# Kernel tuning notes

Hardware: AMD Instinct MI355X
Metric: run time of the kernel (lower is better)

The kernel has to match this reference:

```python
import jax, jax.numpy as jnp
import numpy as np

EMBED_DIM = 512
NUM_HEADS = 8
HEAD_DIM = EMBED_DIM // NUM_HEADS
PAIR_DIM = 64
B, L = 2, 1024


def setup_inputs() -> dict:
    key = jax.random.key(0)
    ks = jax.random.split(key, 6)
    seq_repr = jax.random.normal(ks[0], (B, L, EMBED_DIM), dtype=jnp.float32)
    pair_repr = jax.random.normal(ks[1], (B, L, L, PAIR_DIM), dtype=jnp.float32)
    # Parameters (stored as [in, out] for x @ W)
    sc = 0.02
    W_qkv = jax.random.normal(ks[2], (EMBED_DIM, 3 * EMBED_DIM), dtype=jnp.float32) * sc
    W_bias = jax.random.normal(ks[3], (PAIR_DIM, NUM_HEADS), dtype=jnp.float32) * sc
    W_out = jax.random.normal(ks[4], (EMBED_DIM, EMBED_DIM), dtype=jnp.float32) * sc
    b_out = jax.random.normal(ks[5], (EMBED_DIM,), dtype=jnp.float32) * sc
    return {"seq_repr": seq_repr, "pair_repr": pair_repr,
            "W_qkv": W_qkv, "W_bias": W_bias, "W_out": W_out, "b_out": b_out}


def reference(seq_repr, pair_repr, W_qkv, W_bias, W_out, b_out):
    b, l, _ = seq_repr.shape
    # pair bias: [B, L, L, pair_dim] -> [B, H, L, L]
    pair_bias = jnp.einsum('bijp,ph->bhij', pair_repr, W_bias)
    qkv = seq_repr @ W_qkv                      # [B, L, 3*E]
    q, k, v = jnp.split(qkv, 3, axis=-1)
    def heads(x):
        return x.reshape(b, l, NUM_HEADS, HEAD_DIM).transpose(0, 2, 1, 3)  # [B,H,L,D]
    q, k, v = heads(q), heads(k), heads(v)
    scale = 1.0 / jnp.sqrt(jnp.asarray(HEAD_DIM, dtype=q.dtype))
    scores = jnp.einsum('bhid,bhjd->bhij', q, k) * scale + pair_bias
    attn = jax.nn.softmax(scores, axis=-1)
    ctx = jnp.einsum('bhij,bhjd->bhid', attn, v)             # [B,H,L,D]
    ctx = ctx.transpose(0, 2, 1, 3).reshape(b, l, EMBED_DIM)
    return ctx @ W_out + b_out
```

## Files before the change

### kernel.cpp

```cpp
#include <hip/hip_runtime.h>
#include <hip/hip_bf16.h>


typedef __attribute__((ext_vector_type(8))) short bf16x8;
typedef __attribute__((ext_vector_type(4))) float f32x4;

#define BFLO(u) __uint_as_float(((unsigned)(u)) << 16)

__device__ __forceinline__ unsigned pk2(float a, float b) {
    __hip_bfloat16 ha = __float2bfloat16(a);
    __hip_bfloat16 hb = __float2bfloat16(b);
    return (unsigned)__bfloat16_as_ushort(ha) | ((unsigned)__bfloat16_as_ushort(hb) << 16);
}

__device__ __forceinline__ void gl16_nt(const void* g, void* l) {
    __builtin_amdgcn_global_load_lds((const __attribute__((address_space(1))) void*)g,
                                     (__attribute__((address_space(3))) void*)l, 16, 0, 2);
}

__global__ __launch_bounds__(256, 2) void gemm_qkv_kernel(
    const float* __restrict__ A, const float* __restrict__ W,
    unsigned short* __restrict__ qbus, unsigned short* __restrict__ kbus,
    unsigned short* __restrict__ vtbus)
{
    __shared__ float smem[64 * 68];
    float* As = smem;
    float* Bs = smem + 32 * 68;

    const int t  = threadIdx.x;
    const int m0 = blockIdx.y * 64;
    const int n0 = blockIdx.x * 64;
    const int tx = t & 15, ty = t >> 4;

    const int am = t >> 2, ak = (t & 3) * 8;
    const int bk = t >> 3, bn = (t & 7) * 8;

    float acc[4][4] = {};

    for (int k0 = 0; k0 < 512; k0 += 32) {
        float4 a0 = *(const float4*)&A[(size_t)(m0 + am) * 512 + k0 + ak];
        float4 a1 = *(const float4*)&A[(size_t)(m0 + am) * 512 + k0 + ak + 4];
        float4 b0 = *(const float4*)&W[(size_t)(k0 + bk) * 1536 + n0 + bn];
        float4 b1 = *(const float4*)&W[(size_t)(k0 + bk) * 1536 + n0 + bn + 4];
        __syncthreads();
        As[(ak + 0) * 68 + am] = a0.x;
        As[(ak + 1) * 68 + am] = a0.y;
        As[(ak + 2) * 68 + am] = a0.z;
        As[(ak + 3) * 68 + am] = a0.w;
        As[(ak + 4) * 68 + am] = a1.x;
        As[(ak + 5) * 68 + am] = a1.y;
        As[(ak + 6) * 68 + am] = a1.z;
        As[(ak + 7) * 68 + am] = a1.w;
        *(float4*)&Bs[bk * 68 + bn]     = b0;
        *(float4*)&Bs[bk * 68 + bn + 4] = b1;
        __syncthreads();
#pragma unroll
        for (int kk = 0; kk < 32; kk++) {
            float4 a4 = *(float4*)&As[kk * 68 + ty * 4];
            float4 b4 = *(float4*)&Bs[kk * 68 + tx * 4];
            float av[4] = {a4.x, a4.y, a4.z, a4.w};
            float bv[4] = {b4.x, b4.y, b4.z, b4.w};
#pragma unroll
            for (int r = 0; r < 4; r++)
#pragma unroll
                for (int c = 0; c < 4; c++) acc[r][c] += av[r] * bv[c];
        }
    }

    const int sect = n0 >> 9;
    const int h    = (n0 >> 6) & 7;
    const int b    = m0 >> 10;
    const int i0   = m0 & 1023;

    if (sect == 2) {
        __syncthreads();
        float* T = smem;
#pragma unroll
        for (int r = 0; r < 4; r++)
#pragma unroll
            for (int c = 0; c < 4; c++)
                T[(tx * 4 + c) * 68 + (ty * 4 + r)] = acc[r][c];
        __syncthreads();
        const int dp = t >> 2, iq = (t & 3) * 16;
        unsigned short* dst = vtbus + (((size_t)(b * 8 + h)) * 64 + dp) * 1024 + i0 + iq;
#pragma unroll
        for (int u = 0; u < 4; u++) {
            float4 f = *(float4*)&T[dp * 68 + iq + u * 4];
            uint2 pkd; pkd.x = pk2(f.x, f.y); pkd.y = pk2(f.z, f.w);
            *(uint2*)&dst[u * 4] = pkd;
        }
    } else {
        unsigned short* dst = (sect == 0) ? qbus : kbus;
        const float sc = (sect == 0) ? 0.125f : 1.0f;
#pragma unroll
        for (int r = 0; r < 4; r++) {
            const int i = i0 + ty * 4 + r;
#pragma unroll
            for (int c = 0; c < 4; c += 2) {
                unsigned u = pk2(acc[r][c] * sc, acc[r][c + 1] * sc);
                *(unsigned*)&dst[(((size_t)(b * 8 + h)) * 1024 + i) * 64 + tx * 4 + c] = u;
            }
        }
    }
}

__device__ __forceinline__ bf16x8 slab_frag(const char* rowb, int ks, int q4, int sw) {
    const int s0 = ks * 8 + q4 * 2;
    const float4 fa = *(const float4*)(rowb + (((s0    ) ^ sw) << 4));
    const float4 fb = *(const float4*)(rowb + (((s0 + 1) ^ sw) << 4));
    uint4 u;
    u.x = pk2(fa.x, fa.y); u.y = pk2(fa.z, fa.w);
    u.z = pk2(fb.x, fb.y); u.w = pk2(fb.z, fb.w);
    return *(bf16x8*)&u;
}

__global__ __launch_bounds__(512, 4) void attn_kernel(
    const float* __restrict__ pair, const float* __restrict__ Wb,
    const unsigned short* __restrict__ qbus, const unsigned short* __restrict__ kbus,
    const unsigned short* __restrict__ vtbus, float* __restrict__ cp,
    float* __restrict__ mlm, float* __restrict__ mll)
{
    __shared__ __align__(16) char plds[2][32768];
    __shared__ __align__(16) unsigned short bias_lds[128 * 17];
    __shared__ __align__(16) unsigned short pbuf[8 * 16 * 24];

    const int t    = threadIdx.x;
    const int lane = t & 63;
    const int w    = t >> 6;
    const int q4   = lane >> 4;
    const int l15  = lane & 15;

    const int bx   = blockIdx.x;
    const int vbid = ((bx & 7) << 6) | (bx >> 3);
    const int b    = vbid >> 8;
    const int rem  = vbid & 255;
    const int jh   = rem >> 7;
    const int i0   = (rem & 127) * 8;

    uint4 wbf[2];
#pragma unroll
    for (int ks = 0; ks < 2; ks++) {
        float f[8];
#pragma unroll
        for (int e = 0; e < 8; e++)
            f[e] = (l15 < 8) ? Wb[(ks * 32 + q4 * 8 + e) * 8 + l15] : 0.f;
        wbf[ks].x = pk2(f[0], f[1]); wbf[ks].y = pk2(f[2], f[3]);
        wbf[ks].z = pk2(f[4], f[5]); wbf[ks].w = pk2(f[6], f[7]);
    }

    uint4 qf[2] = {};
    if (l15 < 8) {
        const unsigned short* qrow = qbus + (size_t)((b * 8 + w) * 1024 + i0 + l15) * 64;
#pragma unroll
        for (int ks = 0; ks < 2; ks++)
            qf[ks] = *(const uint4*)(qrow + ks * 32 + q4 * 8);
    }

    asm volatile("s_waitcnt vmcnt(0)" ::: "memory");
    __builtin_amdgcn_sched_barrier(0);

    const char* prow = (const char*)pair
                     + ((size_t)(b * 1024 + i0 + w) * 1024 + jh * 512) * 256;
    int soff[4];
#pragma unroll
    for (int r = 0; r < 4; r++) {
        const int jl = r * 4 + q4;
        soff[r] = jl * 256 + ((l15 ^ jl) << 4);
    }
    char* ldsW = (char*)plds + w * 4096;

#define STAGE(bufsel, jtn) do {                                         \
        const char* gg = prow + (size_t)(jtn) * 4096;                   \
        char* ld = ldsW + (bufsel) * 32768;                             \
        _Pragma("unroll")                                               \
        for (int r = 0; r < 4; r++)                                     \
            gl16_nt(gg + soff[r], ld + r * 1024);                       \
    } while (0)

    STAGE(0, 0);

    f32x4 acc[4];
#pragma unroll
    for (int dn = 0; dn < 4; dn++) acc[dn] = (f32x4){0.f, 0.f, 0.f, 0.f};
    float mrun[4], lrun[4];
#pragma unroll
    for (int rr = 0; rr < 4; rr++) { mrun[rr] = -3.0e38f; lrun[rr] = 0.f; }

    const unsigned short* kbase = kbus + (size_t)((b * 8 + w) * 1024 + jh * 512) * 64;
    const unsigned short* vbase = vtbus + (size_t)((b * 8 + w) * 64) * 1024 + jh * 512;

#pragma unroll 1
    for (int jt = 0; jt < 32; jt++) {
        const char* cur = (const char*)plds + (jt & 1) * 32768;

        uint4 kf[2], vf[4];
        {
            const unsigned short* kt = kbase + (size_t)(jt * 16 + l15) * 64;
            kf[0] = *(const uint4*)(kt + q4 * 8);
            kf[1] = *(const uint4*)(kt + 32 + q4 * 8);
#pragma unroll
            for (int dn = 0; dn < 4; dn++)
                vf[dn] = *(const uint4*)(vbase + (size_t)(dn * 16 + l15) * 1024
                                         + jt * 16 + (q4 & 1) * 8);
        }

        if (jt < 31) {
            STAGE((jt + 1) & 1, jt + 1);
            asm volatile("s_waitcnt vmcnt(10)" ::: "memory");
        } else {
            asm volatile("s_waitcnt vmcnt(6)" ::: "memory");
        }
        __builtin_amdgcn_sched_barrier(0);

        {
            const char* rowb = cur + w * 4096 + l15 * 256;
            f32x4 bb = {0.f, 0.f, 0.f, 0.f};
#pragma unroll
            for (int ks = 0; ks < 2; ks++)
                bb = __builtin_amdgcn_mfma_f32_16x16x32_bf16(
                        slab_frag(rowb, ks, q4, l15), *(bf16x8*)&wbf[ks], bb, 0, 0, 0);
            if (l15 < 8) {
#pragma unroll
                for (int rr = 0; rr < 4; rr++)
                    bias_lds[(w * 16 + q4 * 4 + rr) * 17 + l15] =
                        __bfloat16_as_ushort(__float2bfloat16(bb[rr]));
            }
        }

        asm volatile("s_waitcnt lgkmcnt(0)" ::: "memory");
        __builtin_amdgcn_sched_barrier(0);
        __builtin_amdgcn_s_barrier();
        __builtin_amdgcn_sched_barrier(0);

        f32x4 s;
#pragma unroll
        for (int rr = 0; rr < 4; rr++) {
            const int ii = q4 * 4 + rr;
            s[rr] = (q4 < 2) ? BFLO(bias_lds[(ii * 16 + l15) * 17 + w]) : 0.f;
        }
        s = __builtin_amdgcn_mfma_f32_16x16x32_bf16(*(bf16x8*)&qf[0], *(bf16x8*)&kf[0], s, 0, 0, 0);
        s = __builtin_amdgcn_mfma_f32_16x16x32_bf16(*(bf16x8*)&qf[1], *(bf16x8*)&kf[1], s, 0, 0, 0);

#pragma unroll
        for (int rr = 0; rr < 4; rr++) {
            float x = s[rr];
            x = fmaxf(x, __shfl_xor(x, 1));
            x = fmaxf(x, __shfl_xor(x, 2));
            x = fmaxf(x, __shfl_xor(x, 4));
            x = fmaxf(x, __shfl_xor(x, 8));
            const float mnew = fmaxf(mrun[rr], x);
            const float corr = __expf(mrun[rr] - mnew);
            mrun[rr] = mnew;
            const float p0 = __expf(s[rr] - mnew);
            float ts = p0;
            ts += __shfl_xor(ts, 1);
            ts += __shfl_xor(ts, 2);
            ts += __shfl_xor(ts, 4);
            ts += __shfl_xor(ts, 8);
            lrun[rr] = lrun[rr] * corr + ts;
#pragma unroll
            for (int dn = 0; dn < 4; dn++) acc[dn][rr] *= corr;
            pbuf[(w * 16 + q4 * 4 + rr) * 24 + l15] =
                __bfloat16_as_ushort(__float2bfloat16(p0));
        }

        asm volatile("s_waitcnt lgkmcnt(0)" ::: "memory");
        __builtin_amdgcn_sched_barrier(0);

        bf16x8 pfrag = (bf16x8){0, 0, 0, 0, 0, 0, 0, 0};
        if (q4 < 2) pfrag = *(bf16x8*)&pbuf[(w * 16 + l15) * 24 + q4 * 8];
#pragma unroll
        for (int dn = 0; dn < 4; dn++)
            acc[dn] = __builtin_amdgcn_mfma_f32_16x16x32_bf16(pfrag, *(bf16x8*)&vf[dn], acc[dn], 0, 0, 0);

        __builtin_amdgcn_s_barrier();
    }

    if (q4 < 2) {
#pragma unroll
        for (int rr = 0; rr < 4; rr++) {
            const int i = q4 * 4 + rr;
            float* crow = cp + (size_t)jh * (2048 * 512)
                        + ((size_t)(b * 1024) + i0 + i) * 512 + w * 64;
#pragma unroll
            for (int dn = 0; dn < 4; dn++)
                crow[dn * 16 + l15] = acc[dn][rr];
            if (l15 == 0) {
                const int mi = ((jh * 2 + b) * 8 + w) * 1024 + i0 + i;
                mlm[mi] = mrun[rr];
                mll[mi] = lrun[rr];
            }
        }
    }
#undef STAGE
}

__global__ __launch_bounds__(256, 2) void gemm_out_fused(
    const float* __restrict__ cp, const float* __restrict__ mlm,
    const float* __restrict__ mll, const float* __restrict__ W,
    const float* __restrict__ bias, float* __restrict__ out)
{
    __shared__ float smem[64 * 68];
    float* As = smem;
    float* Bs = smem + 32 * 68;

    const int t  = threadIdx.x;
    const int m0 = blockIdx.y * 64;
    const int n0 = blockIdx.x * 64;
    const int tx = t & 15, ty = t >> 4;

    const int am = t >> 2, ak = (t & 3) * 8;
    const int bk = t >> 3, bn = (t & 7) * 8;

    const int row = m0 + am;
    const int bb  = row >> 10, ii = row & 1023;
    const float* cp0 = cp + (size_t)row * 512;
    const float* cp1 = cp + (size_t)(2048 * 512) + (size_t)row * 512;

    float acc[4][4] = {};
    float w0 = 0.f, w1 = 0.f;

    for (int k0 = 0; k0 < 512; k0 += 32) {
        if ((k0 & 63) == 0) {
            const int h   = k0 >> 6;
            const int mi0 = ((bb) * 8 + h) * 1024 + ii;
            const int mi1 = ((2 + bb) * 8 + h) * 1024 + ii;
            const float m0_ = mlm[mi0], m1_ = mlm[mi1];
            const float l0_ = mll[mi0], l1_ = mll[mi1];
            const float M   = fmaxf(m0_, m1_);
            float e0 = __expf(m0_ - M), e1 = __expf(m1_ - M);
            const float inv = 1.0f / (l0_ * e0 + l1_ * e1);
            w0 = e0 * inv; w1 = e1 * inv;
        }
        float4 c0a = *(const float4*)&cp0[k0 + ak];
        float4 c0b = *(const float4*)&cp0[k0 + ak + 4];
        float4 c1a = *(const float4*)&cp1[k0 + ak];
        float4 c1b = *(const float4*)&cp1[k0 + ak + 4];
        float4 b0 = *(const float4*)&W[(size_t)(k0 + bk) * 512 + n0 + bn];
        float4 b1 = *(const float4*)&W[(size_t)(k0 + bk) * 512 + n0 + bn + 4];
        float a0x = c0a.x * w0 + c1a.x * w1, a0y = c0a.y * w0 + c1a.y * w1;
        float a0z = c0a.z * w0 + c1a.z * w1, a0w = c0a.w * w0 + c1a.w * w1;
        float a1x = c0b.x * w0 + c1b.x * w1, a1y = c0b.y * w0 + c1b.y * w1;
        float a1z = c0b.z * w0 + c1b.z * w1, a1w = c0b.w * w0 + c1b.w * w1;
        __syncthreads();
        As[(ak + 0) * 68 + am] = a0x;
        As[(ak + 1) * 68 + am] = a0y;
        As[(ak + 2) * 68 + am] = a0z;
        As[(ak + 3) * 68 + am] = a0w;
        As[(ak + 4) * 68 + am] = a1x;
        As[(ak + 5) * 68 + am] = a1y;
        As[(ak + 6) * 68 + am] = a1z;
        As[(ak + 7) * 68 + am] = a1w;
        *(float4*)&Bs[bk * 68 + bn]     = b0;
        *(float4*)&Bs[bk * 68 + bn + 4] = b1;
        __syncthreads();
#pragma unroll
        for (int kk = 0; kk < 32; kk++) {
            float4 a4 = *(float4*)&As[kk * 68 + ty * 4];
            float4 b4 = *(float4*)&Bs[kk * 68 + tx * 4];
            float av[4] = {a4.x, a4.y, a4.z, a4.w};
            float bv[4] = {b4.x, b4.y, b4.z, b4.w};
#pragma unroll
            for (int r = 0; r < 4; r++)
#pragma unroll
                for (int c = 0; c < 4; c++) acc[r][c] += av[r] * bv[c];
        }
    }

    float4 bo = *(const float4*)&bias[n0 + tx * 4];
    float bv[4] = {bo.x, bo.y, bo.z, bo.w};
#pragma unroll
    for (int r = 0; r < 4; r++) {
        const int m = m0 + ty * 4 + r;
#pragma unroll
        for (int c = 0; c < 4; c++)
            out[(size_t)m * 512 + n0 + tx * 4 + c] = acc[r][c] + bv[c];
    }
}

extern "C" void kernel_launch(void* const* d_in, const int* in_sizes, int n_in,
                              void* d_out, int out_size, void* d_ws, size_t ws_size,
                              hipStream_t stream)
{
    const float* seq  = (const float*)d_in[0];
    const float* pair = (const float*)d_in[1];
    const float* Wqkv = (const float*)d_in[2];
    const float* Wb   = (const float*)d_in[3];
    const float* Wout = (const float*)d_in[4];
    const float* bout = (const float*)d_in[5];
    float* out = (float*)d_out;

    unsigned short* qbus  = (unsigned short*)d_ws;
    unsigned short* kbus  = qbus + (1 << 20);
    unsigned short* vtbus = kbus + (1 << 20);
    float*          cp    = (float*)(vtbus + (1 << 20));
    float*          mlm   = cp + (2 << 20);
    float*          mll   = mlm + (1 << 15);

    gemm_qkv_kernel<<<dim3(24, 32), 256, 0, stream>>>(seq, Wqkv, qbus, kbus, vtbus);
    attn_kernel<<<512, 512, 0, stream>>>(pair, Wb, qbus, kbus, vtbus, cp, mlm, mll);
    gemm_out_fused<<<dim3(8, 32), 256, 0, stream>>>(cp, mlm, mll, Wout, bout, out);
}
```

Measured before the change: 239.3 us.

## Use bf16 MFMA for QKV projection and pipeline pair-bias computation one tile ahead

Adds a prep kernel that converts seq to bf16 and transposes W_qkv into bf16 [N,K] layout. The QKV GEMM is rewritten to use 16x16x32 bf16 MFMA loading fragments straight from global memory, replacing the fp32 FMA LDS-tiled loop. The attention kernel now stages pair tiles two steps ahead and computes the pair bias for the next tile into a double-buffered LDS slot, which removes one barrier per iteration. The costs are an extra kernel launch with a conversion pass, more workspace, and lower precision in the projection.

```diff
diff --git a/kernel.cpp b/kernel.cpp
--- a/kernel.cpp
+++ b/kernel.cpp
@@ -18,53 +18,83 @@
                                      (__attribute__((address_space(3))) void*)l, 16, 0, 2);
 }
 
-__global__ __launch_bounds__(256, 2) void gemm_qkv_kernel(
-    const float* __restrict__ A, const float* __restrict__ W,
+__global__ __launch_bounds__(256) void prep_kernel(
+    const float* __restrict__ seq, const float* __restrict__ W,
+    unsigned short* __restrict__ seqb, unsigned short* __restrict__ wtb)
+{
+    __shared__ float T[64 * 68];
+    const int bx = blockIdx.x, t = threadIdx.x;
+    if (bx < 512) {
+        const size_t idx = ((size_t)bx * 256 + t) * 8;
+        float4 f0 = *(const float4*)&seq[idx];
+        float4 f1 = *(const float4*)&seq[idx + 4];
+        uint4 u;
+        u.x = pk2(f0.x, f0.y); u.y = pk2(f0.z, f0.w);
+        u.z = pk2(f1.x, f1.y); u.w = pk2(f1.z, f1.w);
+        *(uint4*)&seqb[idx] = u;
+    } else {
+        const int bb = bx - 512;
+        const int n0 = (bb % 24) * 64, k0 = (bb / 24) * 64;
+        const int kk = t >> 2, nch = (t & 3) * 16;
+#pragma unroll
+        for (int u = 0; u < 4; u++) {
+            float4 f = *(const float4*)&W[(size_t)(k0 + kk) * 1536 + n0 + nch + u * 4];
+            T[kk * 68 + nch + u * 4 + 0] = f.x;
+            T[kk * 68 + nch + u * 4 + 1] = f.y;
+            T[kk * 68 + nch + u * 4 + 2] = f.z;
+            T[kk * 68 + nch + u * 4 + 3] = f.w;
+        }
+        __syncthreads();
+        const int nn = t >> 2, kch = (t & 3) * 16;
+#pragma unroll
+        for (int u = 0; u < 4; u++) {
+            float a = T[(kch + u * 4 + 0) * 68 + nn];
+            float b = T[(kch + u * 4 + 1) * 68 + nn];
+            float c = T[(kch + u * 4 + 2) * 68 + nn];
+            float d = T[(kch + u * 4 + 3) * 68 + nn];
+            uint2 p; p.x = pk2(a, b); p.y = pk2(c, d);
+            *(uint2*)&wtb[(size_t)(n0 + nn) * 512 + k0 + kch + u * 4] = p;
+        }
+    }
+}
+
+__global__ __launch_bounds__(256) void gemm_qkv_kernel(
+    const unsigned short* __restrict__ seqb, const unsigned short* __restrict__ wtb,
     unsigned short* __restrict__ qbus, unsigned short* __restrict__ kbus,
     unsigned short* __restrict__ vtbus)
 {
-    __shared__ float smem[64 * 68];
-    float* As = smem;
-    float* Bs = smem + 32 * 68;
-
-    const int t  = threadIdx.x;
+    const int t    = threadIdx.x;
+    const int lane = t & 63;
+    const int wv   = t >> 6;
+    const int q4   = lane >> 4;
+    const int l15  = lane & 15;
+    const int mw   = wv >> 1, nw = wv & 1;
+
     const int m0 = blockIdx.y * 64;
     const int n0 = blockIdx.x * 64;
-    const int tx = t & 15, ty = t >> 4;
-
-    const int am = t >> 2, ak = (t & 3) * 8;
-    const int bk = t >> 3, bn = (t & 7) * 8;
-
-    float acc[4][4] = {};
-
+
+    f32x4 acc[2][2];
+#pragma unroll
+    for (int a = 0; a < 2; a++)
+#pragma unroll
+        for (int b = 0; b < 2; b++) acc[a][b] = (f32x4){0.f, 0.f, 0.f, 0.f};
+
+    const unsigned short* arow0 = seqb + (size_t)(m0 + mw * 32 + l15) * 512 + q4 * 8;
+    const unsigned short* brow0 = wtb + (size_t)(n0 + nw * 32 + l15) * 512 + q4 * 8;
+
+#pragma unroll 4
     for (int k0 = 0; k0 < 512; k0 += 32) {
-        float4 a0 = *(const float4*)&A[(size_t)(m0 + am) * 512 + k0 + ak];
-        float4 a1 = *(const float4*)&A[(size_t)(m0 + am) * 512 + k0 + ak + 4];
-        float4 b0 = *(const float4*)&W[(size_t)(k0 + bk) * 1536 + n0 + bn];
-        float4 b1 = *(const float4*)&W[(size_t)(k0 + bk) * 1536 + n0 + bn + 4];
-        __syncthreads();
-        As[(ak + 0) * 68 + am] = a0.x;
-        As[(ak + 1) * 68 + am] = a0.y;
-        As[(ak + 2) * 68 + am] = a0.z;
-        As[(ak + 3) * 68 + am] = a0.w;
-        As[(ak + 4) * 68 + am] = a1.x;
-        As[(ak + 5) * 68 + am] = a1.y;
-        As[(ak + 6) * 68 + am] = a1.z;
-        As[(ak + 7) * 68 + am] = a1.w;
-        *(float4*)&Bs[bk * 68 + bn]     = b0;
-        *(float4*)&Bs[bk * 68 + bn + 4] = b1;
-        __syncthreads();
-#pragma unroll
-        for (int kk = 0; kk < 32; kk++) {
-            float4 a4 = *(float4*)&As[kk * 68 + ty * 4];
-            float4 b4 = *(float4*)&Bs[kk * 68 + tx * 4];
-            float av[4] = {a4.x, a4.y, a4.z, a4.w};
-            float bv[4] = {b4.x, b4.y, b4.z, b4.w};
-#pragma unroll
-            for (int r = 0; r < 4; r++)
-#pragma unroll
-                for (int c = 0; c < 4; c++) acc[r][c] += av[r] * bv[c];
-        }
+        uint4 af[2], bf[2];
+        af[0] = *(const uint4*)(arow0 + k0);
+        af[1] = *(const uint4*)(arow0 + 16 * 512 + k0);
+        bf[0] = *(const uint4*)(brow0 + k0);
+        bf[1] = *(const uint4*)(brow0 + 16 * 512 + k0);
+#pragma unroll
+        for (int sm = 0; sm < 2; sm++)
+#pragma unroll
+            for (int sn = 0; sn < 2; sn++)
+                acc[sm][sn] = __builtin_amdgcn_mfma_f32_16x16x32_bf16(
+                    *(bf16x8*)&af[sm], *(bf16x8*)&bf[sn], acc[sm][sn], 0, 0, 0);
     }
 
     const int sect = n0 >> 9;
@@ -72,33 +102,24 @@
     const int b    = m0 >> 10;
     const int i0   = m0 & 1023;
 
-    if (sect == 2) {
-        __syncthreads();
-        float* T = smem;
-#pragma unroll
-        for (int r = 0; r < 4; r++)
-#pragma unroll
-            for (int c = 0; c < 4; c++)
-                T[(tx * 4 + c) * 68 + (ty * 4 + r)] = acc[r][c];
-        __syncthreads();
-        const int dp = t >> 2, iq = (t & 3) * 16;
-        unsigned short* dst = vtbus + (((size_t)(b * 8 + h)) * 64 + dp) * 1024 + i0 + iq;
-#pragma unroll
-        for (int u = 0; u < 4; u++) {
-            float4 f = *(float4*)&T[dp * 68 + iq + u * 4];
-            uint2 pkd; pkd.x = pk2(f.x, f.y); pkd.y = pk2(f.z, f.w);
-            *(uint2*)&dst[u * 4] = pkd;
-        }
-    } else {
-        unsigned short* dst = (sect == 0) ? qbus : kbus;
-        const float sc = (sect == 0) ? 0.125f : 1.0f;
-#pragma unroll
-        for (int r = 0; r < 4; r++) {
-            const int i = i0 + ty * 4 + r;
-#pragma unroll
-            for (int c = 0; c < 4; c += 2) {
-                unsigned u = pk2(acc[r][c] * sc, acc[r][c + 1] * sc);
-                *(unsigned*)&dst[(((size_t)(b * 8 + h)) * 1024 + i) * 64 + tx * 4 + c] = u;
+#pragma unroll
+    for (int sm = 0; sm < 2; sm++) {
+#pragma unroll
+        for (int sn = 0; sn < 2; sn++) {
+            const int d  = nw * 32 + sn * 16 + l15;
+            const int ib = i0 + mw * 32 + sm * 16 + q4 * 4;
+            if (sect == 2) {
+                uint2 p;
+                p.x = pk2(acc[sm][sn][0], acc[sm][sn][1]);
+                p.y = pk2(acc[sm][sn][2], acc[sm][sn][3]);
+                *(uint2*)&vtbus[(((size_t)(b * 8 + h)) * 64 + d) * 1024 + ib] = p;
+            } else {
+                unsigned short* dst = (sect == 0) ? qbus : kbus;
+                const float sc = (sect == 0) ? 0.125f : 1.0f;
+#pragma unroll
+                for (int rr = 0; rr < 4; rr++)
+                    dst[(((size_t)(b * 8 + h)) * 1024 + ib + rr) * 64 + d] =
+                        __bfloat16_as_ushort(__float2bfloat16(acc[sm][sn][rr] * sc));
             }
         }
     }
@@ -121,7 +142,7 @@
     float* __restrict__ mlm, float* __restrict__ mll)
 {
     __shared__ __align__(16) char plds[2][32768];
-    __shared__ __align__(16) unsigned short bias_lds[128 * 17];
+    __shared__ __align__(16) unsigned short bias_lds[2][128 * 17];
     __shared__ __align__(16) unsigned short pbuf[8 * 16 * 24];
 
     const int t    = threadIdx.x;
@@ -177,7 +198,32 @@
             gl16_nt(gg + soff[r], ld + r * 1024);                       \
     } while (0)
 
+#define BIASCOMP(pbsel, slot) do {                                      \
+        const char* rowb = (const char*)plds + (pbsel) * 32768          \
+                         + w * 4096 + l15 * 256;                        \
+        f32x4 bb = {0.f, 0.f, 0.f, 0.f};                                \
+        _Pragma("unroll")                                               \
+        for (int ks = 0; ks < 2; ks++)                                  \
+            bb = __builtin_amdgcn_mfma_f32_16x16x32_bf16(               \
+                    slab_frag(rowb, ks, q4, l15), *(bf16x8*)&wbf[ks],   \
+                    bb, 0, 0, 0);                                       \
+        if (l15 < 8) {                                                  \
+            _Pragma("unroll")                                           \
+            for (int rr = 0; rr < 4; rr++)                              \
+                bias_lds[slot][(w * 16 + q4 * 4 + rr) * 17 + l15] =     \
+                    __bfloat16_as_ushort(__float2bfloat16(bb[rr]));     \
+        }                                                               \
+    } while (0)
+
     STAGE(0, 0);
+    STAGE(1, 1);
+    asm volatile("s_waitcnt vmcnt(4)" ::: "memory");
+    __builtin_amdgcn_sched_barrier(0);
+    BIASCOMP(0, 0);
+    asm volatile("s_waitcnt lgkmcnt(0)" ::: "memory");
+    __builtin_amdgcn_sched_barrier(0);
+    __builtin_amdgcn_s_barrier();
+    __builtin_amdgcn_sched_barrier(0);
 
     f32x4 acc[4];
 #pragma unroll
@@ -191,8 +237,6 @@
 
 #pragma unroll 1
     for (int jt = 0; jt < 32; jt++) {
-        const char* cur = (const char*)plds + (jt & 1) * 32768;
-
         uint4 kf[2], vf[4];
         {
             const unsigned short* kt = kbase + (size_t)(jt * 16 + l15) * 64;
@@ -204,39 +248,22 @@
                                          + jt * 16 + (q4 & 1) * 8);
         }
 
-        if (jt < 31) {
-            STAGE((jt + 1) & 1, jt + 1);
+        if (jt < 30) {
+            STAGE(jt & 1, jt + 2);
             asm volatile("s_waitcnt vmcnt(10)" ::: "memory");
-        } else {
+            __builtin_amdgcn_sched_barrier(0);
+            BIASCOMP((jt + 1) & 1, (jt + 1) & 1);
+        } else if (jt == 30) {
             asm volatile("s_waitcnt vmcnt(6)" ::: "memory");
-        }
-        __builtin_amdgcn_sched_barrier(0);
-
-        {
-            const char* rowb = cur + w * 4096 + l15 * 256;
-            f32x4 bb = {0.f, 0.f, 0.f, 0.f};
-#pragma unroll
-            for (int ks = 0; ks < 2; ks++)
-                bb = __builtin_amdgcn_mfma_f32_16x16x32_bf16(
-                        slab_frag(rowb, ks, q4, l15), *(bf16x8*)&wbf[ks], bb, 0, 0, 0);
-            if (l15 < 8) {
-#pragma unroll
-                for (int rr = 0; rr < 4; rr++)
-                    bias_lds[(w * 16 + q4 * 4 + rr) * 17 + l15] =
-                        __bfloat16_as_ushort(__float2bfloat16(bb[rr]));
-            }
-        }
-
-        asm volatile("s_waitcnt lgkmcnt(0)" ::: "memory");
-        __builtin_amdgcn_sched_barrier(0);
-        __builtin_amdgcn_s_barrier();
-        __builtin_amdgcn_sched_barrier(0);
+            __builtin_amdgcn_sched_barrier(0);
+            BIASCOMP(1, 1);
+        }
 
         f32x4 s;
 #pragma unroll
         for (int rr = 0; rr < 4; rr++) {
             const int ii = q4 * 4 + rr;
-            s[rr] = (q4 < 2) ? BFLO(bias_lds[(ii * 16 + l15) * 17 + w]) : 0.f;
+            s[rr] = (q4 < 2) ? BFLO(bias_lds[jt & 1][(ii * 16 + l15) * 17 + w]) : 0.f;
         }
         s = __builtin_amdgcn_mfma_f32_16x16x32_bf16(*(bf16x8*)&qf[0], *(bf16x8*)&kf[0], s, 0, 0, 0);
         s = __builtin_amdgcn_mfma_f32_16x16x32_bf16(*(bf16x8*)&qf[1], *(bf16x8*)&kf[1], s, 0, 0, 0);
@@ -273,7 +300,10 @@
         for (int dn = 0; dn < 4; dn++)
             acc[dn] = __builtin_amdgcn_mfma_f32_16x16x32_bf16(pfrag, *(bf16x8*)&vf[dn], acc[dn], 0, 0, 0);
 
+        asm volatile("s_waitcnt lgkmcnt(0)" ::: "memory");
+        __builtin_amdgcn_sched_barrier(0);
         __builtin_amdgcn_s_barrier();
+        __builtin_amdgcn_sched_barrier(0);
     }
 
     if (q4 < 2) {
@@ -293,6 +323,7 @@
         }
     }
 #undef STAGE
+#undef BIASCOMP
 }
 
 __global__ __launch_bounds__(256, 2) void gemm_out_fused(
@@ -393,11 +424,14 @@
     unsigned short* qbus  = (unsigned short*)d_ws;
     unsigned short* kbus  = qbus + (1 << 20);
     unsigned short* vtbus = kbus + (1 << 20);
-    float*          cp    = (float*)(vtbus + (1 << 20));
+    unsigned short* seqb  = vtbus + (1 << 20);
+    unsigned short* wtb   = seqb + (1 << 20);
+    float*          cp    = (float*)(wtb + (1 << 20));
     float*          mlm   = cp + (2 << 20);
     float*          mll   = mlm + (1 << 15);
 
-    gemm_qkv_kernel<<<dim3(24, 32), 256, 0, stream>>>(seq, Wqkv, qbus, kbus, vtbus);
+    prep_kernel<<<704, 256, 0, stream>>>(seq, Wqkv, seqb, wtb);
+    gemm_qkv_kernel<<<dim3(24, 32), 256, 0, stream>>>(seqb, wtb, qbus, kbus, vtbus);
     attn_kernel<<<512, 512, 0, stream>>>(pair, Wb, qbus, kbus, vtbus, cp, mlm, mll);
     gemm_out_fused<<<dim3(8, 32), 256, 0, stream>>>(cp, mlm, mll, Wout, bout, out);
 }
```

Result: faster. 232.9 us, median of 2 (-2.7%).
